# Kernel optimization log

Measured on AMD Instinct MI355X. Metric: run time of the kernel, lower is better.

Reference implementation:

```python
import jax, jax.numpy as jnp
import numpy as np

EPS = 1e-5  # BatchNorm eps

def setup_inputs() -> dict:
    key = jax.random.key(0)
    ks = jax.random.split(key, 16)
    B, N, C = 8, 4096, 192
    H = C * 4  # dim * mlp_ratio
    scale = 0.02
    return {
        "x":  jax.random.normal(ks[0], (B, N, C), dtype=jnp.float32),
        # fc1: Conv1d(C->H, k=1, bias=False) weight squeezed to [H, C]
        "W1": jax.random.normal(ks[1], (H, C), dtype=jnp.float32) * (1.0 / np.sqrt(C)),
        # BatchNorm1d(H) eval-mode params
        "g1": jax.random.uniform(ks[2], (H,), dtype=jnp.float32, minval=0.5, maxval=1.5),
        "b1": jax.random.normal(ks[3], (H,), dtype=jnp.float32) * 0.1,
        "m1": jax.random.normal(ks[4], (H,), dtype=jnp.float32) * 0.1,
        "v1": jax.random.uniform(ks[5], (H,), dtype=jnp.float32, minval=0.5, maxval=1.5),
        # frequency-domain complex per-channel mixing params (full matrices; einsum uses diagonal)
        "r":  jax.random.normal(ks[6], (H, H), dtype=jnp.float32) * scale,
        "i":  jax.random.normal(ks[7], (H, H), dtype=jnp.float32) * scale,
        "rb": jax.random.normal(ks[8], (H,), dtype=jnp.float32) * scale,
        "ib": jax.random.normal(ks[9], (H,), dtype=jnp.float32) * scale,
        # fc2: Conv1d(H->C, k=1, bias=False) weight squeezed to [C, H]
        "W2": jax.random.normal(ks[10], (C, H), dtype=jnp.float32) * (1.0 / np.sqrt(H)),
        "g2": jax.random.uniform(ks[11], (C,), dtype=jnp.float32, minval=0.5, maxval=1.5),
        "b2": jax.random.normal(ks[12], (C,), dtype=jnp.float32) * 0.1,
        "m2": jax.random.normal(ks[13], (C,), dtype=jnp.float32) * 0.1,
        "v2": jax.random.uniform(ks[14], (C,), dtype=jnp.float32, minval=0.5, maxval=1.5),
    }

def _bn(x, g, b, m, v):
    # eval-mode BatchNorm1d applied on channel (last) axis
    return (x - m) * (g / jnp.sqrt(v + EPS)) + b

def reference(x, W1, g1, b1, m1, v1, r, i, rb, ib, W2, g2, b2, m2, v2):
    # fc1: 1x1 conv over channels + BN + ReLU  -> [B, N, H]
    h = jax.nn.relu(_bn(jnp.einsum('bnc,hc->bnh', x, W1), g1, b1, m1, v1))
    # FFT along token axis (ortho norm)
    xf = jnp.fft.fft(h.astype(jnp.complex64), axis=1, norm='ortho')
    # torch.einsum('bnc,cc->bnc') == per-channel scale by diag of the matrix
    xr = jax.nn.relu(jnp.einsum('bnc,cc->bnc', xf.real, r)
                     - jnp.einsum('bnc,cc->bnc', xf.imag, i) + rb)
    xi = jax.nn.relu(jnp.einsum('bnc,cc->bnc', xf.imag, r)
                     + jnp.einsum('bnc,cc->bnc', xf.real, i) + ib)
    h = jnp.fft.ifft(xr + 1j * xi, axis=1, norm='ortho').real.astype(jnp.float32)
    # fc2: 1x1 conv + BN -> [B, N, C]
    y = _bn(jnp.einsum('bnh,ch->bnc', h, W2), g2, b2, m2, v2)
    return y
```

## Files before the change

### kernel.cpp

```cpp
#include <hip/hip_runtime.h>

typedef float f32x4 __attribute__((ext_vector_type(4)));
typedef __bf16 v8bf __attribute__((ext_vector_type(8)));
typedef unsigned int u32x2 __attribute__((ext_vector_type(2)));

#define B_ 8
#define N_ 4096
#define C_ 192
#define H_ 768

__device__ __forceinline__ unsigned short f2bf(float f) {
  unsigned int u = __float_as_uint(f);
  u += 0x7FFFu + ((u >> 16) & 1u);
  return (unsigned short)(u >> 16);
}
__device__ __forceinline__ unsigned int pk2(float lo, float hi) {
  return (unsigned int)f2bf(lo) | ((unsigned int)f2bf(hi) << 16);
}
__device__ __forceinline__ void unpk(unsigned int w, float& a, float& b) {
  a = __uint_as_float(w << 16);
  b = __uint_as_float(w & 0xFFFF0000u);
}

#define LDS_AS(p) ((__attribute__((address_space(3))) unsigned int*)(void*)(p))
__device__ __forceinline__ void gld16(const void* g, void* l) {
  __builtin_amdgcn_global_load_lds((const __attribute__((address_space(1))) unsigned int*)g,
                                   LDS_AS(l), 16, 0, 0);
}
__device__ __forceinline__ unsigned ldsoff(const void* p) {
  return (unsigned)(size_t)((__attribute__((address_space(3))) char*)(void*)p);
}

__global__ __launch_bounds__(256) void gemm1k(
    const float* __restrict__ x, const float* __restrict__ W1,
    const float* __restrict__ g1, const float* __restrict__ b1,
    const float* __restrict__ m1, const float* __restrict__ v1,
    unsigned short* __restrict__ hb) {
  __shared__ __align__(16) unsigned short pool[18432];
  unsigned short* As = pool;
  unsigned short* Bs = pool + 9216;
  unsigned short* Ts = pool;
  const int n0 = blockIdx.x << 7, h0 = blockIdx.y << 7, b = blockIdx.z;
  const int tid = threadIdx.x;
  const int l = tid & 63, q = l >> 4, l16 = l & 15;
  const int wv = tid >> 6, wr = wv >> 1, wc = wv & 1;
  const int srow = tid >> 3, scol = (tid & 7) << 3;
  f32x4 acc[4][4];
#pragma unroll
  for (int i_ = 0; i_ < 4; ++i_)
#pragma unroll
    for (int j_ = 0; j_ < 4; ++j_) acc[i_][j_] = {0.f, 0.f, 0.f, 0.f};

  for (int kt = 0; kt < 3; ++kt) {
    const int c0 = kt << 6;
#pragma unroll
    for (int p = 0; p < 4; ++p) {
      int row = srow + (p << 5);
      const float4* sa = reinterpret_cast<const float4*>(
          &x[(size_t)(b * N_ + n0 + row) * C_ + c0 + scol]);
      float4 a0 = sa[0], a1 = sa[1];
      uint4 w;
      w.x = pk2(a0.x, a0.y); w.y = pk2(a0.z, a0.w);
      w.z = pk2(a1.x, a1.y); w.w = pk2(a1.z, a1.w);
      *reinterpret_cast<uint4*>(&As[row * 72 + scol]) = w;
      const float4* sb = reinterpret_cast<const float4*>(
          &W1[(size_t)(h0 + row) * C_ + c0 + scol]);
      float4 b0 = sb[0], b1_ = sb[1];
      uint4 u;
      u.x = pk2(b0.x, b0.y); u.y = pk2(b0.z, b0.w);
      u.z = pk2(b1_.x, b1_.y); u.w = pk2(b1_.z, b1_.w);
      *reinterpret_cast<uint4*>(&Bs[row * 72 + scol]) = u;
    }
    __syncthreads();
#pragma unroll
    for (int ks = 0; ks < 2; ++ks) {
      v8bf av[4], bv[4];
#pragma unroll
      for (int f = 0; f < 4; ++f)
        av[f] = *reinterpret_cast<const v8bf*>(&As[((wr << 6) + (f << 4) + l16) * 72 + (ks << 5) + (q << 3)]);
#pragma unroll
      for (int f = 0; f < 4; ++f)
        bv[f] = *reinterpret_cast<const v8bf*>(&Bs[((wc << 6) + (f << 4) + l16) * 72 + (ks << 5) + (q << 3)]);
#pragma unroll
      for (int fm = 0; fm < 4; ++fm)
#pragma unroll
        for (int fn = 0; fn < 4; ++fn)
          acc[fm][fn] = __builtin_amdgcn_mfma_f32_16x16x32_bf16(av[fm], bv[fn], acc[fm][fn], 0, 0, 0);
    }
    __syncthreads();
  }
#pragma unroll
  for (int fn = 0; fn < 4; ++fn) {
    int hl = (wc << 6) + (fn << 4) + l16;
    int hh = h0 + hl;
    float s = g1[hh] * rsqrtf(v1[hh] + 1e-5f);
    float bias = b1[hh] - m1[hh] * s;
#pragma unroll
    for (int fm = 0; fm < 4; ++fm) {
      int nl = (wr << 6) + (fm << 4) + (q << 2);
      ushort4 o;
      o.x = f2bf(fmaxf(acc[fm][fn][0] * s + bias, 0.f));
      o.y = f2bf(fmaxf(acc[fm][fn][1] * s + bias, 0.f));
      o.z = f2bf(fmaxf(acc[fm][fn][2] * s + bias, 0.f));
      o.w = f2bf(fmaxf(acc[fm][fn][3] * s + bias, 0.f));
      *reinterpret_cast<ushort4*>(&Ts[hl * 136 + nl]) = o;
    }
  }
  __syncthreads();
  {
    const int rq = tid >> 4, ch = (tid & 15) << 3;
#pragma unroll
    for (int p = 0; p < 8; ++p) {
      int r = (p << 4) + rq;
      uint4 v = *reinterpret_cast<const uint4*>(&Ts[r * 136 + ch]);
      *reinterpret_cast<uint4*>(&hb[((size_t)(b * H_ + h0 + r) << 12) + n0 + ch]) = v;
    }
  }
}

template <bool INV>
__device__ __forceinline__ void dft4(float& ar, float& ai, float& br, float& bi,
                                     float& cr, float& ci, float& dr, float& di) {
  float t0r = ar + cr, t0i = ai + ci;
  float t1r = ar - cr, t1i = ai - ci;
  float t2r = br + dr, t2i = bi + di;
  float t3r = br - dr, t3i = bi - di;
  ar = t0r + t2r; ai = t0i + t2i;
  cr = t0r - t2r; ci = t0i - t2i;
  if (!INV) { br = t1r + t3i; bi = t1i - t3r; dr = t1r - t3i; di = t1i + t3r; }
  else      { br = t1r - t3i; bi = t1i + t3r; dr = t1r + t3i; di = t1i - t3r; }
}
template <bool INV>
__device__ __forceinline__ void twc(float& xr, float& xi, float wr, float wi) {
  float iw = INV ? -wi : wi;
  float nr = xr * wr - xi * iw;
  xi = xr * iw + xi * wr;
  xr = nr;
}
template <bool INV>
__device__ __forceinline__ void fft16(float* xr, float* xi) {
#pragma unroll
  for (int j = 0; j < 4; ++j)
    dft4<INV>(xr[j], xi[j], xr[j + 4], xi[j + 4], xr[j + 8], xi[j + 8], xr[j + 12], xi[j + 12]);
  const float C1 = 0.9238795325112867f, S1 = -0.3826834323650898f;
  const float C2 = 0.7071067811865476f, S2 = -0.7071067811865476f;
  twc<INV>(xr[5], xi[5], C1, S1);
  twc<INV>(xr[6], xi[6], C2, S2);
  twc<INV>(xr[9], xi[9], C2, S2);
  twc<INV>(xr[7], xi[7], -S1, -C1);
  twc<INV>(xr[13], xi[13], -S1, -C1);
  twc<INV>(xr[10], xi[10], 0.f, -1.f);
  twc<INV>(xr[11], xi[11], -C2, S2);
  twc<INV>(xr[14], xi[14], -C2, S2);
  twc<INV>(xr[15], xi[15], -C1, -S1);
  float yr[16], yi[16];
#pragma unroll
  for (int k = 0; k < 4; ++k) {
    float ar = xr[4 * k], ai = xi[4 * k], br = xr[4 * k + 1], bi = xi[4 * k + 1];
    float cr = xr[4 * k + 2], ci = xi[4 * k + 2], dr = xr[4 * k + 3], di = xi[4 * k + 3];
    dft4<INV>(ar, ai, br, bi, cr, ci, dr, di);
    yr[k] = ar; yi[k] = ai; yr[k + 4] = br; yi[k + 4] = bi;
    yr[k + 8] = cr; yi[k + 8] = ci; yr[k + 12] = dr; yi[k + 12] = di;
  }
#pragma unroll
  for (int qq = 0; qq < 16; ++qq) { xr[qq] = yr[qq]; xi[qq] = yi[qq]; }
}
template <bool INV>
__device__ __forceinline__ void fft8(float* xr, float* xi) {
  float er[4] = {xr[0], xr[2], xr[4], xr[6]}, ei[4] = {xi[0], xi[2], xi[4], xi[6]};
  float o_r[4] = {xr[1], xr[3], xr[5], xr[7]}, o_i[4] = {xi[1], xi[3], xi[5], xi[7]};
  dft4<INV>(er[0], ei[0], er[1], ei[1], er[2], ei[2], er[3], ei[3]);
  dft4<INV>(o_r[0], o_i[0], o_r[1], o_i[1], o_r[2], o_i[2], o_r[3], o_i[3]);
  const float c = 0.7071067811865476f;
  twc<INV>(o_r[1], o_i[1], c, -c);
  twc<INV>(o_r[2], o_i[2], 0.f, -1.f);
  twc<INV>(o_r[3], o_i[3], -c, -c);
#pragma unroll
  for (int k = 0; k < 4; ++k) {
    xr[k] = er[k] + o_r[k]; xi[k] = ei[k] + o_i[k];
    xr[k + 4] = er[k] - o_r[k]; xi[k + 4] = ei[k] - o_i[k];
  }
}
template <bool INV>
__device__ __forceinline__ void twchain(float* xr, float* xi, int j, float invL) {
  float ang = -6.283185307179586f * (float)j * invL;
  if (INV) ang = -ang;
  float s1, c1;
  __sincosf(ang, &s1, &c1);
  float wr = c1, wi = s1;
#pragma unroll
  for (int r2 = 1; r2 < 16; ++r2) {
    float nr = xr[r2] * wr - xi[r2] * wi;
    xi[r2] = xr[r2] * wi + xi[r2] * wr;
    xr[r2] = nr;
    float t2 = wr * c1 - wi * s1;
    wi = wr * s1 + wi * c1;
    wr = t2;
  }
}

__device__ __forceinline__ void mixpair(float2 Zk, float2 Zp, float wr, float wi,
                                        float dr, float di, float rbh, float ibh,
                                        float2& G1, float2& G2) {
  const float sc = 0.015625f;
  float Er = 0.5f * (Zk.x + Zp.x), Ei = 0.5f * (Zk.y - Zp.y);
  float Or = 0.5f * (Zk.y + Zp.y), Oi = 0.5f * (Zp.x - Zk.x);
  float WOr = wr * Or - wi * Oi, WOi = wr * Oi + wi * Or;
  float X1r = Er + WOr, X1i = Ei + WOi;
  float X2r = Er - WOr, X2i = Ei - WOi;
  float p1 = dr * X1r * sc, p2 = di * X1i * sc, p3 = dr * X1i * sc, p4 = di * X1r * sc;
  float y1r = fmaxf(p1 - p2 + rbh, 0.f), y1i = fmaxf(p3 + p4 + ibh, 0.f);
  float y4r = fmaxf(p1 + p2 + rbh, 0.f), y4i = fmaxf(p4 - p3 + ibh, 0.f);
  float q1 = dr * X2r * sc, q2 = di * X2i * sc, q3 = dr * X2i * sc, q4 = di * X2r * sc;
  float y2r = fmaxf(q1 - q2 + rbh, 0.f), y2i = fmaxf(q3 + q4 + ibh, 0.f);
  float y3r = fmaxf(q1 + q2 + rbh, 0.f), y3i = fmaxf(q4 - q3 + ibh, 0.f);
  float Hkr = 0.5f * (y1r + y4r), Hki = 0.5f * (y1i - y4i);
  float H2r = 0.5f * (y2r + y3r), H2i = 0.5f * (y2i - y3i);
  float Sr = Hkr + H2r, Si = Hki + H2i;
  float Dr = Hkr - H2r, Di = Hki - H2i;
  float P = wi * Dr - wr * Di, Q = wr * Dr + wi * Di;
  G1 = make_float2(Sr + P, Si + Q);
  G2 = make_float2(Sr - P, Q - Si);
}

#define PIDX(i) ((i) + ((i) >> 4))
__global__ __launch_bounds__(256) void fftmixk(
    unsigned short* __restrict__ hb, const float* __restrict__ Rm,
    const float* __restrict__ Im, const float* __restrict__ rb,
    const float* __restrict__ ib) {
  __shared__ float2 cxs[4352];
  const int b = blockIdx.y;
  const int tid = threadIdx.x;
  const int ch = tid >> 7, j = tid & 127;
  const int h = (blockIdx.x << 1) | ch;
  const int cb = ch * 2176;
  unsigned short* sig = hb + ((size_t)(b * H_ + h) << 12);
  const unsigned int* sig32 = reinterpret_cast<const unsigned int*>(sig);
  unsigned int* o32 = reinterpret_cast<unsigned int*>(sig);

  float xr[16], xi[16];
#pragma unroll
  for (int s = 0; s < 16; ++s) {
    unsigned int w = sig32[j + (s << 7)];
    unpk(w, xr[s], xi[s]);
  }
  fft16<false>(xr, xi);
  twchain<false>(xr, xi, j, 1.0f / 2048.0f);
#pragma unroll
  for (int s = 0; s < 16; ++s) cxs[cb + PIDX(j + (s << 7))] = make_float2(xr[s], xi[s]);
  __syncthreads();
  const int c2 = j >> 3, j2 = j & 7;
#pragma unroll
  for (int s = 0; s < 16; ++s) {
    float2 v = cxs[cb + PIDX((c2 << 7) + j2 + (s << 3))];
    xr[s] = v.x; xi[s] = v.y;
  }
  fft16<false>(xr, xi);
  twchain<false>(xr, xi, j2, 1.0f / 128.0f);
#pragma unroll
  for (int s = 0; s < 16; ++s) cxs[cb + PIDX((c2 << 7) + j2 + (s << 3))] = make_float2(xr[s], xi[s]);
  __syncthreads();
#pragma unroll
  for (int gg = 0; gg < 2; ++gg) {
    int g = j + (gg << 7);
#pragma unroll
    for (int s = 0; s < 8; ++s) {
      float2 v = cxs[cb + PIDX((g << 3) + s)];
      xr[(gg << 3) + s] = v.x; xi[(gg << 3) + s] = v.y;
    }
  }
  __syncthreads();
#pragma unroll
  for (int gg = 0; gg < 2; ++gg) {
    int g = j + (gg << 7);
    fft8<false>(&xr[gg << 3], &xi[gg << 3]);
    int kb = (g >> 4) + ((g & 15) << 4);
#pragma unroll
    for (int s = 0; s < 8; ++s)
      cxs[cb + PIDX(kb + (s << 8))] = make_float2(xr[(gg << 3) + s], xi[(gg << 3) + s]);
  }
  __syncthreads();
  {
    const float dr = Rm[(size_t)h * (H_ + 1)];
    const float di = Im[(size_t)h * (H_ + 1)];
    const float rbh = rb[h], ibh = ib[h];
    float sn, cs;
    __sincosf(3.14159265358979f * (float)j / 256.0f, &sn, &cs);
    float wr = cs, wi = -sn;
    const float WSR = 0.9999988234517019f, WSI = -0.0015339801862847655f;
#pragma unroll
    for (int u = 0; u < 8; ++u) {
      int k = (j << 3) + u;
      int kp = (2048 - k) & 2047;
      float2 Zk = cxs[cb + PIDX(k)];
      float2 Zp = cxs[cb + PIDX(kp)];
      float2 G1, G2;
      mixpair(Zk, Zp, wr, wi, dr, di, rbh, ibh, G1, G2);
      cxs[cb + PIDX(k)] = G1;
      cxs[cb + PIDX(kp)] = G2;
      float nwr = wr * WSR - wi * WSI;
      wi = wr * WSI + wi * WSR;
      wr = nwr;
    }
    if (j == 0) {
      float2 Zs = cxs[cb + PIDX(1024)];
      float2 G1, G2;
      mixpair(Zs, Zs, 0.f, -1.f, dr, di, rbh, ibh, G1, G2);
      cxs[cb + PIDX(1024)] = G1;
    }
  }
  __syncthreads();
#pragma unroll
  for (int gg = 0; gg < 2; ++gg) {
    int g = j + (gg << 7);
    int kb = (g >> 4) + ((g & 15) << 4);
#pragma unroll
    for (int s = 0; s < 8; ++s) {
      float2 v = cxs[cb + PIDX(kb + (s << 8))];
      xr[(gg << 3) + s] = v.x; xi[(gg << 3) + s] = v.y;
    }
  }
  __syncthreads();
#pragma unroll
  for (int gg = 0; gg < 2; ++gg) {
    int g = j + (gg << 7);
    fft8<true>(&xr[gg << 3], &xi[gg << 3]);
#pragma unroll
    for (int s = 0; s < 8; ++s)
      cxs[cb + PIDX((g << 3) + s)] = make_float2(xr[(gg << 3) + s], xi[(gg << 3) + s]);
  }
  __syncthreads();
#pragma unroll
  for (int s = 0; s < 16; ++s) {
    float2 v = cxs[cb + PIDX((c2 << 7) + j2 + (s << 3))];
    xr[s] = v.x; xi[s] = v.y;
  }
  twchain<true>(xr, xi, j2, 1.0f / 128.0f);
  fft16<true>(xr, xi);
#pragma unroll
  for (int s = 0; s < 16; ++s) cxs[cb + PIDX((c2 << 7) + j2 + (s << 3))] = make_float2(xr[s], xi[s]);
  __syncthreads();
#pragma unroll
  for (int s = 0; s < 16; ++s) {
    float2 v = cxs[cb + PIDX(j + (s << 7))];
    xr[s] = v.x; xi[s] = v.y;
  }
  twchain<true>(xr, xi, j, 1.0f / 2048.0f);
  fft16<true>(xr, xi);
#pragma unroll
  for (int s = 0; s < 16; ++s)
    o32[j + (s << 7)] = pk2(xr[s] * 0.015625f, xi[s] * 0.015625f);
}

__global__ __launch_bounds__(256) void gemm2k(
    const unsigned short* __restrict__ hb, const float* __restrict__ W2,
    const float* __restrict__ g2, const float* __restrict__ b2,
    const float* __restrict__ m2, const float* __restrict__ v2,
    float* __restrict__ out) {
  __shared__ __align__(16) float poolf[8704];
  unsigned short* Asw = (unsigned short*)poolf;
  unsigned short* Bsh = (unsigned short*)poolf + 4608;
  float* Tn = poolf;
  const int n0 = blockIdx.x << 7, c0 = blockIdx.y << 6, b = blockIdx.z;
  const int tid = threadIdx.x;
  const int l = tid & 63, q = l >> 4, l16 = l & 15;
  const int wv = tid >> 6, wn2 = wv >> 1, wc2 = wv & 1;
  const int srow = tid >> 3, scol = (tid & 7) << 3;
  const unsigned bbase = ldsoff(&Bsh[0]);
  f32x4 acc[2][4];
#pragma unroll
  for (int i_ = 0; i_ < 2; ++i_)
#pragma unroll
    for (int j_ = 0; j_ < 4; ++j_) acc[i_][j_] = {0.f, 0.f, 0.f, 0.f};

  for (int kt = 0; kt < 12; ++kt) {
    const int k0 = kt << 6;
#pragma unroll
    for (int p = 0; p < 2; ++p) {
      int row = srow + (p << 5);
      const float4* sa = reinterpret_cast<const float4*>(
          &W2[(size_t)(c0 + row) * H_ + k0 + scol]);
      float4 a0 = sa[0], a1 = sa[1];
      uint4 w;
      w.x = pk2(a0.x, a0.y); w.y = pk2(a0.z, a0.w);
      w.z = pk2(a1.x, a1.y); w.w = pk2(a1.z, a1.w);
      *reinterpret_cast<uint4*>(&Asw[row * 72 + scol]) = w;
    }
#pragma unroll
    for (int p = 0; p < 4; ++p) {
      int s = tid + (p << 8);
      int k = ((s >> 6) << 2) | ((s >> 1) & 3);
      int n = (((s >> 3) & 7) << 4) | ((s & 1) << 3);
      gld16(&hb[((size_t)(b * H_ + k0 + k) << 12) + n0 + n], &Bsh[s << 3]);
    }
    __syncthreads();
    v8bf afr[2][2];
#pragma unroll
    for (int fm = 0; fm < 2; ++fm)
#pragma unroll
      for (int ks = 0; ks < 2; ++ks)
        afr[fm][ks] = *reinterpret_cast<const v8bf*>(
            &Asw[((wc2 << 5) + (fm << 4) + l16) * 72 + (ks << 5) + (q << 3)]);
    u32x2 tr[4][2][2];
#pragma unroll
    for (int fn = 0; fn < 4; ++fn)
#pragma unroll
      for (int ks = 0; ks < 2; ++ks) {
        int nidx = (wn2 << 2) + fn;
        unsigned a = bbase + (unsigned)((l16 << 3) + (q << 11) + (ks << 13) + (nidx << 7));
        asm volatile("ds_read_b64_tr_b16 %0, %1 offset:0" : "=v"(tr[fn][ks][0]) : "v"(a));
        asm volatile("ds_read_b64_tr_b16 %0, %1 offset:1024" : "=v"(tr[fn][ks][1]) : "v"(a));
      }
    asm volatile("s_waitcnt lgkmcnt(0)" ::: "memory");
    __builtin_amdgcn_sched_barrier(0);
#pragma unroll
    for (int ks = 0; ks < 2; ++ks)
#pragma unroll
      for (int fn = 0; fn < 4; ++fn) {
        union { unsigned int u[4]; v8bf v; } bb;
        bb.u[0] = tr[fn][ks][0].x; bb.u[1] = tr[fn][ks][0].y;
        bb.u[2] = tr[fn][ks][1].x; bb.u[3] = tr[fn][ks][1].y;
#pragma unroll
        for (int fm = 0; fm < 2; ++fm)
          acc[fm][fn] = __builtin_amdgcn_mfma_f32_16x16x32_bf16(afr[fm][ks], bb.v, acc[fm][fn], 0, 0, 0);
      }
    __syncthreads();
  }
#pragma unroll
  for (int fm = 0; fm < 2; ++fm) {
    int cl = (wc2 << 5) + (fm << 4) + (q << 2);
    int c4 = c0 + cl;
    float4 gv = *reinterpret_cast<const float4*>(&g2[c4]);
    float4 vv = *reinterpret_cast<const float4*>(&v2[c4]);
    float4 bv = *reinterpret_cast<const float4*>(&b2[c4]);
    float4 mv = *reinterpret_cast<const float4*>(&m2[c4]);
    float4 sc, bi;
    sc.x = gv.x * rsqrtf(vv.x + 1e-5f); bi.x = bv.x - mv.x * sc.x;
    sc.y = gv.y * rsqrtf(vv.y + 1e-5f); bi.y = bv.y - mv.y * sc.y;
    sc.z = gv.z * rsqrtf(vv.z + 1e-5f); bi.z = bv.z - mv.z * sc.z;
    sc.w = gv.w * rsqrtf(vv.w + 1e-5f); bi.w = bv.w - mv.w * sc.w;
#pragma unroll
    for (int fn = 0; fn < 4; ++fn) {
      int nl = (wn2 << 6) + (fn << 4) + l16;
      float4 o;
      o.x = acc[fm][fn][0] * sc.x + bi.x;
      o.y = acc[fm][fn][1] * sc.y + bi.y;
      o.z = acc[fm][fn][2] * sc.z + bi.z;
      o.w = acc[fm][fn][3] * sc.w + bi.w;
      *reinterpret_cast<float4*>(&Tn[nl * 68 + cl]) = o;
    }
  }
  __syncthreads();
  {
    const int rq = tid >> 4, ch = (tid & 15) << 2;
#pragma unroll
    for (int p = 0; p < 8; ++p) {
      int r = (p << 4) + rq;
      float4 v = *reinterpret_cast<const float4*>(&Tn[r * 68 + ch]);
      *reinterpret_cast<float4*>(&out[(size_t)(b * N_ + n0 + r) * C_ + c0 + ch]) = v;
    }
  }
}

extern "C" void kernel_launch(void* const* d_in, const int* in_sizes, int n_in,
                              void* d_out, int out_size, void* d_ws, size_t ws_size,
                              hipStream_t stream) {
  const float* x  = (const float*)d_in[0];
  const float* W1 = (const float*)d_in[1];
  const float* g1 = (const float*)d_in[2];
  const float* b1 = (const float*)d_in[3];
  const float* m1 = (const float*)d_in[4];
  const float* v1 = (const float*)d_in[5];
  const float* Rm = (const float*)d_in[6];
  const float* Im = (const float*)d_in[7];
  const float* rb = (const float*)d_in[8];
  const float* ib = (const float*)d_in[9];
  const float* W2 = (const float*)d_in[10];
  const float* g2 = (const float*)d_in[11];
  const float* b2 = (const float*)d_in[12];
  const float* m2 = (const float*)d_in[13];
  const float* v2 = (const float*)d_in[14];
  float* out = (float*)d_out;

  unsigned short* hb = (unsigned short*)d_ws;

  gemm1k<<<dim3(32, 6, 8), 256, 0, stream>>>(x, W1, g1, b1, m1, v1, hb);
  fftmixk<<<dim3(384, 8), 256, 0, stream>>>(hb, Rm, Im, rb, ib);
  gemm2k<<<dim3(32, 3, 8), 256, 0, stream>>>(hb, W2, g2, b2, m2, v2, out);
}
```

Measured before the change: 203.8 us.

## Fuse last FFT stage with spectral mixing in registers and pad row stride

```diff
diff --git a/kernel.cpp b/kernel.cpp
--- a/kernel.cpp
+++ b/kernel.cpp
@@ -8,6 +8,7 @@
 #define N_ 4096
 #define C_ 192
 #define H_ 768
+#define NP_ 4352
 
 __device__ __forceinline__ unsigned short f2bf(float f) {
   unsigned int u = __float_as_uint(f);
@@ -113,7 +114,7 @@
     for (int p = 0; p < 8; ++p) {
       int r = (p << 4) + rq;
       uint4 v = *reinterpret_cast<const uint4*>(&Ts[r * 136 + ch]);
-      *reinterpret_cast<uint4*>(&hb[((size_t)(b * H_ + h0 + r) << 12) + n0 + ch]) = v;
+      *reinterpret_cast<uint4*>(&hb[(size_t)(b * H_ + h0 + r) * NP_ + n0 + ch]) = v;
     }
   }
 }
@@ -222,6 +223,12 @@
   G1 = make_float2(Sr + P, Si + Q);
   G2 = make_float2(Sr - P, Q - Si);
 }
+__device__ __forceinline__ void rotE8(float& wr, float& wi) {
+  const float ER = 0.9238795325112867f, EI = -0.3826834323650898f;
+  float t = wr * ER - wi * EI;
+  wi = wr * EI + wi * ER;
+  wr = t;
+}
 
 #define PIDX(i) ((i) + ((i) >> 4))
 __global__ __launch_bounds__(256) void fftmixk(
@@ -234,7 +241,7 @@
   const int ch = tid >> 7, j = tid & 127;
   const int h = (blockIdx.x << 1) | ch;
   const int cb = ch * 2176;
-  unsigned short* sig = hb + ((size_t)(b * H_ + h) << 12);
+  unsigned short* sig = hb + (size_t)(b * H_ + h) * NP_;
   const unsigned int* sig32 = reinterpret_cast<const unsigned int*>(sig);
   unsigned int* o32 = reinterpret_cast<unsigned int*>(sig);
 
@@ -260,75 +267,66 @@
 #pragma unroll
   for (int s = 0; s < 16; ++s) cxs[cb + PIDX((c2 << 7) + j2 + (s << 3))] = make_float2(xr[s], xi[s]);
   __syncthreads();
-#pragma unroll
-  for (int gg = 0; gg < 2; ++gg) {
-    int g = j + (gg << 7);
-#pragma unroll
-    for (int s = 0; s < 8; ++s) {
-      float2 v = cxs[cb + PIDX((g << 3) + s)];
-      xr[(gg << 3) + s] = v.x; xi[(gg << 3) + s] = v.y;
-    }
-  }
-  __syncthreads();
-#pragma unroll
-  for (int gg = 0; gg < 2; ++gg) {
-    int g = j + (gg << 7);
-    fft8<false>(&xr[gg << 3], &xi[gg << 3]);
-    int kb = (g >> 4) + ((g & 15) << 4);
-#pragma unroll
-    for (int s = 0; s < 8; ++s)
-      cxs[cb + PIDX(kb + (s << 8))] = make_float2(xr[(gg << 3) + s], xi[(gg << 3) + s]);
-  }
-  __syncthreads();
+  int gA, gB;
+  if (j == 0)       { gA = 0;       gB = 8;       }
+  else if (j < 8)   { gA = j;       gB = 16 - j;  }
+  else if (j < 16)  { gA = 120 + j; gB = 151 - j; }
+  else              { gA = j;       gB = 271 - j; }
+  const int pA = cb + (gA << 3) + (gA >> 1);
+  const int pB = cb + (gB << 3) + (gB >> 1);
+#pragma unroll
+  for (int t = 0; t < 8; ++t) { float2 v = cxs[pA + t]; xr[t] = v.x; xi[t] = v.y; }
+#pragma unroll
+  for (int t = 0; t < 8; ++t) { float2 v = cxs[pB + t]; xr[8 + t] = v.x; xi[8 + t] = v.y; }
+  fft8<false>(xr, xi);
+  fft8<false>(xr + 8, xi + 8);
   {
     const float dr = Rm[(size_t)h * (H_ + 1)];
     const float di = Im[(size_t)h * (H_ + 1)];
     const float rbh = rb[h], ibh = ib[h];
-    float sn, cs;
-    __sincosf(3.14159265358979f * (float)j / 256.0f, &sn, &cs);
-    float wr = cs, wi = -sn;
-    const float WSR = 0.9999988234517019f, WSI = -0.0015339801862847655f;
-#pragma unroll
-    for (int u = 0; u < 8; ++u) {
-      int k = (j << 3) + u;
-      int kp = (2048 - k) & 2047;
-      float2 Zk = cxs[cb + PIDX(k)];
-      float2 Zp = cxs[cb + PIDX(kp)];
-      float2 G1, G2;
-      mixpair(Zk, Zp, wr, wi, dr, di, rbh, ibh, G1, G2);
-      cxs[cb + PIDX(k)] = G1;
-      cxs[cb + PIDX(kp)] = G2;
-      float nwr = wr * WSR - wi * WSI;
-      wi = wr * WSI + wi * WSR;
-      wr = nwr;
-    }
     if (j == 0) {
-      float2 Zs = cxs[cb + PIDX(1024)];
-      float2 G1, G2;
-      mixpair(Zs, Zs, 0.f, -1.f, dr, di, rbh, ibh, G1, G2);
-      cxs[cb + PIDX(1024)] = G1;
-    }
-  }
-  __syncthreads();
-#pragma unroll
-  for (int gg = 0; gg < 2; ++gg) {
-    int g = j + (gg << 7);
-    int kb = (g >> 4) + ((g & 15) << 4);
-#pragma unroll
-    for (int s = 0; s < 8; ++s) {
-      float2 v = cxs[cb + PIDX(kb + (s << 8))];
-      xr[(gg << 3) + s] = v.x; xi[(gg << 3) + s] = v.y;
-    }
-  }
-  __syncthreads();
-#pragma unroll
-  for (int gg = 0; gg < 2; ++gg) {
-    int g = j + (gg << 7);
-    fft8<true>(&xr[gg << 3], &xi[gg << 3]);
-#pragma unroll
-    for (int s = 0; s < 8; ++s)
-      cxs[cb + PIDX((g << 3) + s)] = make_float2(xr[(gg << 3) + s], xi[(gg << 3) + s]);
-  }
+      float wr = 1.f, wi = 0.f;
+#pragma unroll
+      for (int m3 = 0; m3 <= 4; ++m3) {
+        int p = (8 - m3) & 7;
+        float2 G1, G2;
+        mixpair(make_float2(xr[m3], xi[m3]), make_float2(xr[p], xi[p]),
+                wr, wi, dr, di, rbh, ibh, G1, G2);
+        xr[m3] = G1.x; xi[m3] = G1.y; xr[p] = G2.x; xi[p] = G2.y;
+        rotE8(wr, wi);
+      }
+      wr = 0.9807852804032304f; wi = -0.19509032201612825f;
+#pragma unroll
+      for (int m3 = 0; m3 < 4; ++m3) {
+        int p = 15 - m3;
+        float2 G1, G2;
+        mixpair(make_float2(xr[8 + m3], xi[8 + m3]), make_float2(xr[p], xi[p]),
+                wr, wi, dr, di, rbh, ibh, G1, G2);
+        xr[8 + m3] = G1.x; xi[8 + m3] = G1.y; xr[p] = G2.x; xi[p] = G2.y;
+        rotE8(wr, wi);
+      }
+    } else {
+      int kbA = (gA >> 4) + ((gA & 15) << 4);
+      float sn, cs;
+      __sincosf((float)kbA * 1.5339807878856412e-3f, &sn, &cs);
+      float wr = cs, wi = -sn;
+#pragma unroll
+      for (int m3 = 0; m3 < 8; ++m3) {
+        int p = 15 - m3;
+        float2 G1, G2;
+        mixpair(make_float2(xr[m3], xi[m3]), make_float2(xr[p], xi[p]),
+                wr, wi, dr, di, rbh, ibh, G1, G2);
+        xr[m3] = G1.x; xi[m3] = G1.y; xr[p] = G2.x; xi[p] = G2.y;
+        rotE8(wr, wi);
+      }
+    }
+  }
+  fft8<true>(xr, xi);
+  fft8<true>(xr + 8, xi + 8);
+#pragma unroll
+  for (int t = 0; t < 8; ++t) cxs[pA + t] = make_float2(xr[t], xi[t]);
+#pragma unroll
+  for (int t = 0; t < 8; ++t) cxs[pB + t] = make_float2(xr[8 + t], xi[8 + t]);
   __syncthreads();
 #pragma unroll
   for (int s = 0; s < 16; ++s) {
@@ -391,7 +389,7 @@
       int s = tid + (p << 8);
       int k = ((s >> 6) << 2) | ((s >> 1) & 3);
       int n = (((s >> 3) & 7) << 4) | ((s & 1) << 3);
-      gld16(&hb[((size_t)(b * H_ + k0 + k) << 12) + n0 + n], &Bsh[s << 3]);
+      gld16(&hb[(size_t)(b * H_ + k0 + k) * NP_ + n0 + n], &Bsh[s << 3]);
     }
     __syncthreads();
     v8bf afr[2][2];
```

Result: no change. 206.0 us (+1.1%).

## Pre-convert inputs to bf16 and double-buffer GEMM tiles via async LDS loads

Applied to the files above, without the earlier changes.

```diff
diff --git a/kernel.cpp b/kernel.cpp
--- a/kernel.cpp
+++ b/kernel.cpp
@@ -31,56 +31,72 @@
   return (unsigned)(size_t)((__attribute__((address_space(3))) char*)(void*)p);
 }
 
+__global__ __launch_bounds__(256) void cvtk(
+    const float* __restrict__ x, const float* __restrict__ w1, const float* __restrict__ w2,
+    unsigned short* __restrict__ xb, unsigned short* __restrict__ w1b,
+    unsigned short* __restrict__ w2b) {
+  int i = blockIdx.x * 256 + threadIdx.x;
+  const float* src; unsigned short* dst; int off;
+  if (i < 786432)      { src = x;  dst = xb;  off = i; }
+  else if (i < 804864) { src = w1; dst = w1b; off = i - 786432; }
+  else                 { src = w2; dst = w2b; off = i - 804864; }
+  const float4* s4 = reinterpret_cast<const float4*>(src + (size_t)off * 8);
+  float4 a = s4[0], b = s4[1];
+  uint4 o;
+  o.x = pk2(a.x, a.y); o.y = pk2(a.z, a.w);
+  o.z = pk2(b.x, b.y); o.w = pk2(b.z, b.w);
+  *reinterpret_cast<uint4*>(dst + (size_t)off * 8) = o;
+}
+
 __global__ __launch_bounds__(256) void gemm1k(
-    const float* __restrict__ x, const float* __restrict__ W1,
+    const unsigned short* __restrict__ xb, const unsigned short* __restrict__ W1b,
     const float* __restrict__ g1, const float* __restrict__ b1,
     const float* __restrict__ m1, const float* __restrict__ v1,
     unsigned short* __restrict__ hb) {
-  __shared__ __align__(16) unsigned short pool[18432];
-  unsigned short* As = pool;
-  unsigned short* Bs = pool + 9216;
+  __shared__ __align__(16) unsigned short pool[32768];
+  char* LB = (char*)pool;
   unsigned short* Ts = pool;
   const int n0 = blockIdx.x << 7, h0 = blockIdx.y << 7, b = blockIdx.z;
   const int tid = threadIdx.x;
   const int l = tid & 63, q = l >> 4, l16 = l & 15;
   const int wv = tid >> 6, wr = wv >> 1, wc = wv & 1;
-  const int srow = tid >> 3, scol = (tid & 7) << 3;
   f32x4 acc[4][4];
 #pragma unroll
   for (int i_ = 0; i_ < 4; ++i_)
 #pragma unroll
     for (int j_ = 0; j_ < 4; ++j_) acc[i_][j_] = {0.f, 0.f, 0.f, 0.f};
 
+  auto STAGE = [&](int kt, int nxt) {
+    const int k0 = kt << 6;
+#pragma unroll
+    for (int p = 0; p < 4; ++p) {
+      int s = tid + (p << 8);
+      int r = s >> 3, cs = s & 7, csl = cs ^ (r & 7);
+      gld16(&xb[(size_t)(b * N_ + n0 + r) * C_ + k0 + (csl << 3)],
+            LB + ((unsigned)nxt << 14) + ((unsigned)s << 4));
+      gld16(&W1b[(size_t)(h0 + r) * C_ + k0 + (csl << 3)],
+            LB + 32768u + ((unsigned)nxt << 14) + ((unsigned)s << 4));
+    }
+  };
+
+  STAGE(0, 0);
+  __syncthreads();
+  int cur = 0;
   for (int kt = 0; kt < 3; ++kt) {
-    const int c0 = kt << 6;
-#pragma unroll
-    for (int p = 0; p < 4; ++p) {
-      int row = srow + (p << 5);
-      const float4* sa = reinterpret_cast<const float4*>(
-          &x[(size_t)(b * N_ + n0 + row) * C_ + c0 + scol]);
-      float4 a0 = sa[0], a1 = sa[1];
-      uint4 w;
-      w.x = pk2(a0.x, a0.y); w.y = pk2(a0.z, a0.w);
-      w.z = pk2(a1.x, a1.y); w.w = pk2(a1.z, a1.w);
-      *reinterpret_cast<uint4*>(&As[row * 72 + scol]) = w;
-      const float4* sb = reinterpret_cast<const float4*>(
-          &W1[(size_t)(h0 + row) * C_ + c0 + scol]);
-      float4 b0 = sb[0], b1_ = sb[1];
-      uint4 u;
-      u.x = pk2(b0.x, b0.y); u.y = pk2(b0.z, b0.w);
-      u.z = pk2(b1_.x, b1_.y); u.w = pk2(b1_.z, b1_.w);
-      *reinterpret_cast<uint4*>(&Bs[row * 72 + scol]) = u;
-    }
-    __syncthreads();
+    if (kt < 2) STAGE(kt + 1, cur ^ 1);
+    const unsigned aL = (unsigned)cur << 14;
+    const unsigned bL = 32768u + ((unsigned)cur << 14);
 #pragma unroll
     for (int ks = 0; ks < 2; ++ks) {
+      const unsigned jo = ((unsigned)ks << 6) | ((unsigned)q << 4);
       v8bf av[4], bv[4];
 #pragma unroll
-      for (int f = 0; f < 4; ++f)
-        av[f] = *reinterpret_cast<const v8bf*>(&As[((wr << 6) + (f << 4) + l16) * 72 + (ks << 5) + (q << 3)]);
-#pragma unroll
-      for (int f = 0; f < 4; ++f)
-        bv[f] = *reinterpret_cast<const v8bf*>(&Bs[((wc << 6) + (f << 4) + l16) * 72 + (ks << 5) + (q << 3)]);
+      for (int f = 0; f < 4; ++f) {
+        int rowA = (wr << 6) + (f << 4) + l16;
+        av[f] = *reinterpret_cast<const v8bf*>(LB + aL + rowA * 128 + (jo ^ ((rowA & 7) << 4)));
+        int rowB = (wc << 6) + (f << 4) + l16;
+        bv[f] = *reinterpret_cast<const v8bf*>(LB + bL + rowB * 128 + (jo ^ ((rowB & 7) << 4)));
+      }
 #pragma unroll
       for (int fm = 0; fm < 4; ++fm)
 #pragma unroll
@@ -88,6 +104,7 @@
           acc[fm][fn] = __builtin_amdgcn_mfma_f32_16x16x32_bf16(av[fm], bv[fn], acc[fm][fn], 0, 0, 0);
     }
     __syncthreads();
+    cur ^= 1;
   }
 #pragma unroll
   for (int fn = 0; fn < 4; ++fn) {
@@ -353,61 +370,64 @@
 }
 
 __global__ __launch_bounds__(256) void gemm2k(
-    const unsigned short* __restrict__ hb, const float* __restrict__ W2,
+    const unsigned short* __restrict__ hb, const unsigned short* __restrict__ W2b,
     const float* __restrict__ g2, const float* __restrict__ b2,
     const float* __restrict__ m2, const float* __restrict__ v2,
     float* __restrict__ out) {
-  __shared__ __align__(16) float poolf[8704];
-  unsigned short* Asw = (unsigned short*)poolf;
-  unsigned short* Bsh = (unsigned short*)poolf + 4608;
-  float* Tn = poolf;
+  __shared__ __align__(16) unsigned short pool[24576];
+  char* LB = (char*)pool;
+  float* Tn = (float*)pool;
   const int n0 = blockIdx.x << 7, c0 = blockIdx.y << 6, b = blockIdx.z;
   const int tid = threadIdx.x;
   const int l = tid & 63, q = l >> 4, l16 = l & 15;
   const int wv = tid >> 6, wn2 = wv >> 1, wc2 = wv & 1;
-  const int srow = tid >> 3, scol = (tid & 7) << 3;
-  const unsigned bbase = ldsoff(&Bsh[0]);
+  const unsigned lbase = ldsoff(LB);
   f32x4 acc[2][4];
 #pragma unroll
   for (int i_ = 0; i_ < 2; ++i_)
 #pragma unroll
     for (int j_ = 0; j_ < 4; ++j_) acc[i_][j_] = {0.f, 0.f, 0.f, 0.f};
 
-  for (int kt = 0; kt < 12; ++kt) {
+  auto STAGE = [&](int kt, int nxt) {
     const int k0 = kt << 6;
-#pragma unroll
-    for (int p = 0; p < 2; ++p) {
-      int row = srow + (p << 5);
-      const float4* sa = reinterpret_cast<const float4*>(
-          &W2[(size_t)(c0 + row) * H_ + k0 + scol]);
-      float4 a0 = sa[0], a1 = sa[1];
-      uint4 w;
-      w.x = pk2(a0.x, a0.y); w.y = pk2(a0.z, a0.w);
-      w.z = pk2(a1.x, a1.y); w.w = pk2(a1.z, a1.w);
-      *reinterpret_cast<uint4*>(&Asw[row * 72 + scol]) = w;
-    }
 #pragma unroll
     for (int p = 0; p < 4; ++p) {
       int s = tid + (p << 8);
       int k = ((s >> 6) << 2) | ((s >> 1) & 3);
       int n = (((s >> 3) & 7) << 4) | ((s & 1) << 3);
-      gld16(&hb[((size_t)(b * H_ + k0 + k) << 12) + n0 + n], &Bsh[s << 3]);
-    }
-    __syncthreads();
+      gld16(&hb[((size_t)(b * H_ + k0 + k) << 12) + n0 + n], LB + (nxt << 14) + (s << 4));
+    }
+#pragma unroll
+    for (int p = 0; p < 2; ++p) {
+      int s = tid + (p << 8);
+      int r = s >> 3, cs = s & 7, csl = cs ^ (r & 7);
+      gld16(&W2b[(size_t)(c0 + r) * H_ + k0 + (csl << 3)], LB + 32768 + (nxt << 13) + (s << 4));
+    }
+  };
+
+  STAGE(0, 0);
+  __syncthreads();
+  int cur = 0;
+  for (int kt = 0; kt < 12; ++kt) {
+    if (kt < 11) STAGE(kt + 1, cur ^ 1);
+    const unsigned ab = 32768u + ((unsigned)cur << 13);
+    const unsigned bb = (unsigned)cur << 14;
     v8bf afr[2][2];
 #pragma unroll
     for (int fm = 0; fm < 2; ++fm)
 #pragma unroll
-      for (int ks = 0; ks < 2; ++ks)
-        afr[fm][ks] = *reinterpret_cast<const v8bf*>(
-            &Asw[((wc2 << 5) + (fm << 4) + l16) * 72 + (ks << 5) + (q << 3)]);
+      for (int ks = 0; ks < 2; ++ks) {
+        int row = (wc2 << 5) + (fm << 4) + l16;
+        unsigned off = ab + row * 128 + (((ks << 6) | (q << 4)) ^ ((row & 7) << 4));
+        afr[fm][ks] = *reinterpret_cast<const v8bf*>(LB + off);
+      }
     u32x2 tr[4][2][2];
 #pragma unroll
     for (int fn = 0; fn < 4; ++fn)
 #pragma unroll
       for (int ks = 0; ks < 2; ++ks) {
         int nidx = (wn2 << 2) + fn;
-        unsigned a = bbase + (unsigned)((l16 << 3) + (q << 11) + (ks << 13) + (nidx << 7));
+        unsigned a = lbase + bb + (unsigned)((l16 << 3) + (q << 11) + (ks << 13) + (nidx << 7));
         asm volatile("ds_read_b64_tr_b16 %0, %1 offset:0" : "=v"(tr[fn][ks][0]) : "v"(a));
         asm volatile("ds_read_b64_tr_b16 %0, %1 offset:1024" : "=v"(tr[fn][ks][1]) : "v"(a));
       }
@@ -417,14 +437,15 @@
     for (int ks = 0; ks < 2; ++ks)
 #pragma unroll
       for (int fn = 0; fn < 4; ++fn) {
-        union { unsigned int u[4]; v8bf v; } bb;
-        bb.u[0] = tr[fn][ks][0].x; bb.u[1] = tr[fn][ks][0].y;
-        bb.u[2] = tr[fn][ks][1].x; bb.u[3] = tr[fn][ks][1].y;
+        union { unsigned int u[4]; v8bf v; } bbv;
+        bbv.u[0] = tr[fn][ks][0].x; bbv.u[1] = tr[fn][ks][0].y;
+        bbv.u[2] = tr[fn][ks][1].x; bbv.u[3] = tr[fn][ks][1].y;
 #pragma unroll
         for (int fm = 0; fm < 2; ++fm)
-          acc[fm][fn] = __builtin_amdgcn_mfma_f32_16x16x32_bf16(afr[fm][ks], bb.v, acc[fm][fn], 0, 0, 0);
+          acc[fm][fn] = __builtin_amdgcn_mfma_f32_16x16x32_bf16(afr[fm][ks], bbv.v, acc[fm][fn], 0, 0, 0);
       }
     __syncthreads();
+    cur ^= 1;
   }
 #pragma unroll
   for (int fm = 0; fm < 2; ++fm) {
@@ -482,9 +503,13 @@
   const float* v2 = (const float*)d_in[14];
   float* out = (float*)d_out;
 
-  unsigned short* hb = (unsigned short*)d_ws;
-
-  gemm1k<<<dim3(32, 6, 8), 256, 0, stream>>>(x, W1, g1, b1, m1, v1, hb);
+  unsigned short* hb  = (unsigned short*)d_ws;
+  unsigned short* xb  = hb + (size_t)25165824;
+  unsigned short* W1b = xb + (size_t)6291456;
+  unsigned short* W2b = W1b + (size_t)147456;
+
+  cvtk<<<3216, 256, 0, stream>>>(x, W1, W2, xb, W1b, W2b);
+  gemm1k<<<dim3(32, 6, 8), 256, 0, stream>>>(xb, W1b, g1, b1, m1, v1, hb);
   fftmixk<<<dim3(384, 8), 256, 0, stream>>>(hb, Rm, Im, rb, ib);
-  gemm2k<<<dim3(32, 3, 8), 256, 0, stream>>>(hb, W2, g2, b2, m2, v2, out);
-}
+  gemm2k<<<dim3(32, 3, 8), 256, 0, stream>>>(hb, W2b, g2, b2, m2, v2, out);
+}
```

New measurement: 192.1 us. -5.7%, faster.
